# Kernel optimization log

Hardware: AMD Instinct MI355X
Metric: run time of the kernel (lower is better)

## Reference

```python
import jax, jax.numpy as jnp
import numpy as np

DIM_SOL = 8192
DIM_CONTEXT = 2048
DIM_HIDDEN = 4096
INIT = 0.01


def setup_inputs() -> dict:
    key = jax.random.key(0)
    k1, k2, k3, k4, k5, k6 = jax.random.split(key, 6)
    context = jax.random.normal(k1, (DIM_CONTEXT,), dtype=jnp.float32)
    solution = jax.random.randint(k2, (DIM_SOL,), 0, 2).astype(jnp.float32)
    W = jax.random.uniform(k3, (DIM_HIDDEN, DIM_CONTEXT + DIM_SOL), dtype=jnp.float32, minval=-INIT, maxval=INIT)
    U = jax.random.uniform(k4, (DIM_SOL, DIM_HIDDEN), dtype=jnp.float32, minval=-INIT, maxval=INIT)
    b = jax.random.uniform(k5, (DIM_SOL,), dtype=jnp.float32, minval=-INIT, maxval=INIT)
    c = jax.random.uniform(k6, (DIM_HIDDEN,), dtype=jnp.float32, minval=-INIT, maxval=INIT)
    return {"context": context, "solution": solution, "W": W, "U": U, "b": b, "c": c}


def reference(context, solution, W, U, b, c):
    W_ctx = W[:, :DIM_CONTEXT]          # [H, C]
    W_sol = W[:, DIM_CONTEXT:]          # [H, D]
    base = c + W_ctx @ context          # [H]
    # a_i = base + sum_{j<i} W_sol[:, j] * s_j  -> exclusive cumsum over D.
    contrib = W_sol * solution[None, :]                     # [H, D]
    excl = jnp.cumsum(contrib, axis=1) - contrib            # exclusive prefix sum
    A = base[:, None] + excl                                # [H, D]
    H_mat = jax.nn.sigmoid(A.T)                             # [D, H], h at step i
    p_dist = jax.nn.sigmoid(b + jnp.einsum("dh,dh->d", U, H_mat))  # [D]
    # Faithful to source: p_val = prod_i ( p_i^{s_i} + (1 - p_0)^{1 - s_i} )
    terms = jnp.power(p_dist, solution) + jnp.power(1.0 - p_dist[0], 1.0 - solution)
    p_val = jnp.prod(terms)
    return (p_val, p_dist)
```

## Files before the change

### kernel.cpp

```cpp
#include <hip/hip_runtime.h>

#define DSOL 8192
#define DCTX 2048
#define DHID 4096
#define ROWL 10240
#define NSEG 64
#define SEGL 128
#define NCHUNK 16
#define DB 32

typedef float vfloat4 __attribute__((ext_vector_type(4)));

__device__ __forceinline__ float fast_sigmoid(float x) {
    return __builtin_amdgcn_rcpf(1.0f + __expf(-x));
}
__device__ __forceinline__ vfloat4 nt_load4(const float* p) {
    return __builtin_nontemporal_load((const vfloat4*)p);
}

__global__ __launch_bounds__(256) void k_row(
    const float* __restrict__ W, const float* __restrict__ ctx,
    const float* __restrict__ sol, const float* __restrict__ c,
    float* __restrict__ base, float* __restrict__ C)
{
    const int h = blockIdx.x;
    const int t = threadIdx.x;
    const int w = t >> 6, l = t & 63;
    const float* row = W + (size_t)h * ROWL;

    __shared__ float ss[NSEG];
    __shared__ float bred[4];

    float bacc = 0.f;
    #pragma unroll
    for (int i = 0; i < 2; ++i) {
        const int j = i * 1024 + 4 * t;
        const vfloat4 wv = nt_load4(row + j);
        const float4 cv = *(const float4*)(ctx + j);
        bacc += wv.x*cv.x + wv.y*cv.y + wv.z*cv.z + wv.w*cv.w;
    }
    #pragma unroll
    for (int o = 32; o > 0; o >>= 1) bacc += __shfl_xor(bacc, o);
    if (l == 0) bred[w] = bacc;

    const float* rs = row + DCTX;
    #pragma unroll
    for (int i = 0; i < 8; ++i) {
        const int j = i * 1024 + 4 * t;
        const float4 wv = *(const float4*)(rs + j);
        const float4 sv = *(const float4*)(sol + j);
        float a = wv.x*sv.x + wv.y*sv.y + wv.z*sv.z + wv.w*sv.w;
        #pragma unroll
        for (int o = 16; o > 0; o >>= 1) a += __shfl_xor(a, o);
        if ((l & 31) == 0) ss[8*i + 2*w + (l >> 5)] = a;
    }
    __syncthreads();
    if (t == 0) {
        base[h] = c[h] + bred[0] + bred[1] + bred[2] + bred[3];
        float run = 0.f;
        for (int k = 0; k < NSEG; ++k) { const float v = ss[k]; ss[k] = run; run += v; }
    }
    __syncthreads();
    if (t < NSEG) C[t * DHID + h] = ss[t];
}

__global__ __launch_bounds__(256, 4) void k_main(
    const float* __restrict__ W, const float* __restrict__ sol,
    const float* __restrict__ U, const float* __restrict__ base,
    const float* __restrict__ C, float* __restrict__ part)
{
    const int k  = blockIdx.x;
    const int ch = blockIdx.y;
    const int t  = threadIdx.x;
    const int h  = ch * 256 + t;
    const int d0 = k * SEGL;

    __shared__ float T[256][DB + 1];
    __shared__ float sblk[DB];
    __shared__ float R[8][DB];

    float P = C[k * DHID + h];
    const float bs = base[h];

    for (int tb = 0; tb < SEGL / DB; ++tb) {
        const int db0 = d0 + tb * DB;

        {
            int r = t >> 3;
            const int c4 = (t & 7) * 4;
            #pragma unroll
            for (int p = 0; p < 8; ++p, r += 32) {
                const float4 v = *(const float4*)(W + (size_t)(ch*256 + r)*ROWL + DCTX + db0 + c4);
                *(float4*)&T[r][c4] = v;
            }
            if (t < DB) sblk[t] = sol[db0 + t];
        }
        __syncthreads();

        #pragma unroll 8
        for (int d = 0; d < DB; ++d) {
            const float wv = T[t][d];
            const float sg = fast_sigmoid(bs + P);
            const float u  = __builtin_nontemporal_load(U + (size_t)(db0 + d) * DHID + h);
            T[t][d] = u * sg;
            P = fmaf(wv, sblk[d], P);
        }
        __syncthreads();

        {
            const int col = t & 31, g = t >> 5;
            float a = 0.f;
            #pragma unroll
            for (int r = 0; r < 32; ++r) a += T[g*32 + r][col];
            R[g][col] = a;
        }
        __syncthreads();
        if (t < DB) {
            float a = 0.f;
            #pragma unroll
            for (int g = 0; g < 8; ++g) a += R[g][t];
            part[(size_t)ch * DSOL + db0 + t] = a;
        }
        __syncthreads();
    }
}

__global__ __launch_bounds__(256) void k_final(
    const float* __restrict__ b, const float* __restrict__ part,
    const float* __restrict__ sol, float* __restrict__ out,
    float* __restrict__ lsum, float* __restrict__ c0s)
{
    const int t = threadIdx.x;
    const int d = blockIdx.x * 256 + t;
    float acc = b[d];
    #pragma unroll
    for (int cc = 0; cc < NCHUNK; ++cc) acc += part[(size_t)cc * DSOL + d];
    const float p = 1.0f / (1.0f + __expf(-acc));
    out[1 + d] = p;

    const bool one = (sol[d] != 0.0f);
    float lt = one ? __logf(1.0f + p) : 0.0f;
    float c0 = one ? 0.0f : 1.0f;
    #pragma unroll
    for (int o = 32; o > 0; o >>= 1) { lt += __shfl_xor(lt, o); c0 += __shfl_xor(c0, o); }
    __shared__ float rl[4], rc[4];
    if ((t & 63) == 0) { rl[t >> 6] = lt; rc[t >> 6] = c0; }
    __syncthreads();
    if (t == 0) {
        lsum[blockIdx.x] = rl[0] + rl[1] + rl[2] + rl[3];
        c0s [blockIdx.x] = rc[0] + rc[1] + rc[2] + rc[3];
    }
}

__global__ __launch_bounds__(64) void k_tail(
    const float* __restrict__ lsum, const float* __restrict__ c0s,
    float* __restrict__ out)
{
    const int t = threadIdx.x;
    float ls = (t < DSOL/256) ? lsum[t] : 0.0f;
    float c0 = (t < DSOL/256) ? c0s[t]  : 0.0f;
    #pragma unroll
    for (int o = 32; o > 0; o >>= 1) { ls += __shfl_xor(ls, o); c0 += __shfl_xor(c0, o); }
    if (t == 0) {
        const float p0 = out[1];
        const float tot = ls + c0 * __logf(2.0f - p0);
        out[0] = (tot > 88.0f) ? 3.0e38f : __expf(tot);
    }
}

extern "C" void kernel_launch(void* const* d_in, const int* in_sizes, int n_in,
                              void* d_out, int out_size, void* d_ws, size_t ws_size,
                              hipStream_t stream)
{
    const float* ctx = (const float*)d_in[0];
    const float* sol = (const float*)d_in[1];
    const float* W   = (const float*)d_in[2];
    const float* U   = (const float*)d_in[3];
    const float* b   = (const float*)d_in[4];
    const float* c   = (const float*)d_in[5];
    float* out = (float*)d_out;

    float* ws   = (float*)d_ws;
    float* base = ws;
    float* C    = ws + DHID;
    float* part = C + (size_t)NSEG * DHID;
    float* lsum = part + (size_t)NCHUNK * DSOL;
    float* c0s  = lsum + DSOL/256;

    k_row <<<dim3(DHID),         dim3(256), 0, stream>>>(W, ctx, sol, c, base, C);
    k_main<<<dim3(NSEG, NCHUNK), dim3(256), 0, stream>>>(W, sol, U, base, C, part);
    k_final<<<dim3(DSOL / 256),  dim3(256), 0, stream>>>(b, part, sol, out, lsum, c0s);
    k_tail <<<dim3(1),           dim3(64),  0, stream>>>(lsum, c0s, out);
}
```

Measured before the change: 81.11 us.

## Fuse row-prefix kernel into main kernel with per-chunk atomic barrier

Merges the per-row base/segment-prefix computation into the main kernel. Each block computes 4 rows, publishes them, and increments a per-chunk counter. Blocks then spin on the counter until all 64 segments of their chunk are ready. While waiting, each block preloads its first W tile, and later tiles are now prefetched after each step. This removes a kernel launch and overlaps the row pass with tile loads, but it relies on all 1024 blocks being co-resident to avoid deadlock. It also adds a zeroing kernel launch.

```diff
diff --git a/kernel.cpp b/kernel.cpp
--- a/kernel.cpp
+++ b/kernel.cpp
@@ -9,99 +9,103 @@
 #define NCHUNK 16
 #define DB 32
 
-typedef float vfloat4 __attribute__((ext_vector_type(4)));
-
 __device__ __forceinline__ float fast_sigmoid(float x) {
     return __builtin_amdgcn_rcpf(1.0f + __expf(-x));
 }
-__device__ __forceinline__ vfloat4 nt_load4(const float* p) {
-    return __builtin_nontemporal_load((const vfloat4*)p);
-}
-
-__global__ __launch_bounds__(256) void k_row(
+
+__global__ void k_zero(int* __restrict__ cnt) { cnt[threadIdx.x] = 0; }
+
+__global__ __launch_bounds__(256, 4) void k_fused(
     const float* __restrict__ W, const float* __restrict__ ctx,
     const float* __restrict__ sol, const float* __restrict__ c,
-    float* __restrict__ base, float* __restrict__ C)
-{
-    const int h = blockIdx.x;
-    const int t = threadIdx.x;
-    const int w = t >> 6, l = t & 63;
-    const float* row = W + (size_t)h * ROWL;
-
-    __shared__ float ss[NSEG];
-    __shared__ float bred[4];
-
-    float bacc = 0.f;
-    #pragma unroll
-    for (int i = 0; i < 2; ++i) {
-        const int j = i * 1024 + 4 * t;
-        const vfloat4 wv = nt_load4(row + j);
-        const float4 cv = *(const float4*)(ctx + j);
-        bacc += wv.x*cv.x + wv.y*cv.y + wv.z*cv.z + wv.w*cv.w;
-    }
-    #pragma unroll
-    for (int o = 32; o > 0; o >>= 1) bacc += __shfl_xor(bacc, o);
-    if (l == 0) bred[w] = bacc;
-
-    const float* rs = row + DCTX;
-    #pragma unroll
-    for (int i = 0; i < 8; ++i) {
-        const int j = i * 1024 + 4 * t;
-        const float4 wv = *(const float4*)(rs + j);
-        const float4 sv = *(const float4*)(sol + j);
-        float a = wv.x*sv.x + wv.y*sv.y + wv.z*sv.z + wv.w*sv.w;
-        #pragma unroll
-        for (int o = 16; o > 0; o >>= 1) a += __shfl_xor(a, o);
-        if ((l & 31) == 0) ss[8*i + 2*w + (l >> 5)] = a;
-    }
-    __syncthreads();
-    if (t == 0) {
-        base[h] = c[h] + bred[0] + bred[1] + bred[2] + bred[3];
-        float run = 0.f;
-        for (int k = 0; k < NSEG; ++k) { const float v = ss[k]; ss[k] = run; run += v; }
-    }
-    __syncthreads();
-    if (t < NSEG) C[t * DHID + h] = ss[t];
-}
-
-__global__ __launch_bounds__(256, 4) void k_main(
-    const float* __restrict__ W, const float* __restrict__ sol,
-    const float* __restrict__ U, const float* __restrict__ base,
-    const float* __restrict__ C, float* __restrict__ part)
+    const float* __restrict__ U,
+    float* __restrict__ base, float* __restrict__ C,
+    float* __restrict__ part, int* __restrict__ cnt)
 {
     const int k  = blockIdx.x;
     const int ch = blockIdx.y;
     const int t  = threadIdx.x;
-    const int h  = ch * 256 + t;
-    const int d0 = k * SEGL;
-
+    const int w  = t >> 6, l = t & 63;
+
+    __shared__ float ss[4][NSEG];
     __shared__ float T[256][DB + 1];
     __shared__ float sblk[DB];
     __shared__ float R[8][DB];
 
-    float P = C[k * DHID + h];
-    const float bs = base[h];
+    {
+        const int h = ch * 256 + 4 * k + w;
+        const float* row = W + (size_t)h * ROWL;
+
+        float bacc = 0.f;
+        #pragma unroll
+        for (int i = 0; i < 8; ++i) {
+            const int j = i * 256 + l * 4;
+            const float4 wv = *(const float4*)(row + j);
+            const float4 cv = *(const float4*)(ctx + j);
+            bacc += wv.x*cv.x + wv.y*cv.y + wv.z*cv.z + wv.w*cv.w;
+        }
+        #pragma unroll
+        for (int o = 32; o > 0; o >>= 1) bacc += __shfl_xor(bacc, o);
+
+        const float* rs = row + DCTX;
+        #pragma unroll 4
+        for (int g = 0; g < 32; ++g) {
+            const int j = g * 256 + l * 4;
+            const float4 wv = *(const float4*)(rs + j);
+            const float4 sv = *(const float4*)(sol + j);
+            float a = wv.x*sv.x + wv.y*sv.y + wv.z*sv.z + wv.w*sv.w;
+            #pragma unroll
+            for (int o = 16; o > 0; o >>= 1) a += __shfl_xor(a, o);
+            if ((l & 31) == 0) ss[w][2*g + (l >> 5)] = a;
+        }
+        __syncthreads();
+
+        float v = ss[w][l];
+        const float orig = v;
+        #pragma unroll
+        for (int o = 1; o < 64; o <<= 1) {
+            const float u = __shfl_up(v, o);
+            if (l >= o) v += u;
+        }
+        C[(size_t)l * DHID + h] = v - orig;
+        if (l == 0) base[h] = c[h] + bacc;
+    }
+    __threadfence();
+    __syncthreads();
+    if (t == 0)
+        __hip_atomic_fetch_add(&cnt[ch], 1, __ATOMIC_RELEASE, __HIP_MEMORY_SCOPE_AGENT);
+
+    const int h2 = ch * 256 + t;
+    const int d0 = k * SEGL;
+    {
+        int r = t >> 3;
+        const int c4 = (t & 7) * 4;
+        #pragma unroll
+        for (int p = 0; p < 8; ++p, r += 32) {
+            const float4 v = *(const float4*)(W + (size_t)(ch*256 + r)*ROWL + DCTX + d0 + c4);
+            *(float4*)&T[r][c4] = v;
+        }
+        if (t < DB) sblk[t] = sol[d0 + t];
+    }
+
+    for (int spin = 0; spin < (1 << 24); ++spin) {
+        if (__hip_atomic_load(&cnt[ch], __ATOMIC_ACQUIRE, __HIP_MEMORY_SCOPE_AGENT) >= NSEG)
+            break;
+        __builtin_amdgcn_s_sleep(2);
+    }
+    __syncthreads();
+
+    float P = C[(size_t)k * DHID + h2];
+    const float bs = base[h2];
 
     for (int tb = 0; tb < SEGL / DB; ++tb) {
         const int db0 = d0 + tb * DB;
-
-        {
-            int r = t >> 3;
-            const int c4 = (t & 7) * 4;
-            #pragma unroll
-            for (int p = 0; p < 8; ++p, r += 32) {
-                const float4 v = *(const float4*)(W + (size_t)(ch*256 + r)*ROWL + DCTX + db0 + c4);
-                *(float4*)&T[r][c4] = v;
-            }
-            if (t < DB) sblk[t] = sol[db0 + t];
-        }
-        __syncthreads();
 
         #pragma unroll 8
         for (int d = 0; d < DB; ++d) {
             const float wv = T[t][d];
             const float sg = fast_sigmoid(bs + P);
-            const float u  = __builtin_nontemporal_load(U + (size_t)(db0 + d) * DHID + h);
+            const float u  = __builtin_nontemporal_load(U + (size_t)(db0 + d) * DHID + h2);
             T[t][d] = u * sg;
             P = fmaf(wv, sblk[d], P);
         }
@@ -115,11 +119,23 @@
             R[g][col] = a;
         }
         __syncthreads();
+
         if (t < DB) {
             float a = 0.f;
             #pragma unroll
             for (int g = 0; g < 8; ++g) a += R[g][t];
             part[(size_t)ch * DSOL + db0 + t] = a;
+        }
+        if (tb + 1 < SEGL / DB) {
+            const int nb0 = d0 + (tb + 1) * DB;
+            int r = t >> 3;
+            const int c4 = (t & 7) * 4;
+            #pragma unroll
+            for (int p = 0; p < 8; ++p, r += 32) {
+                const float4 v = *(const float4*)(W + (size_t)(ch*256 + r)*ROWL + DCTX + nb0 + c4);
+                *(float4*)&T[r][c4] = v;
+            }
+            if (t < DB) sblk[t] = sol[nb0 + t];
         }
         __syncthreads();
     }
@@ -180,15 +196,16 @@
     const float* c   = (const float*)d_in[5];
     float* out = (float*)d_out;
 
-    float* ws   = (float*)d_ws;
-    float* base = ws;
-    float* C    = ws + DHID;
+    int*   cnt  = (int*)d_ws;
+    float* fws  = (float*)d_ws + 64;
+    float* base = fws;
+    float* C    = base + DHID;
     float* part = C + (size_t)NSEG * DHID;
     float* lsum = part + (size_t)NCHUNK * DSOL;
     float* c0s  = lsum + DSOL/256;
 
-    k_row <<<dim3(DHID),         dim3(256), 0, stream>>>(W, ctx, sol, c, base, C);
-    k_main<<<dim3(NSEG, NCHUNK), dim3(256), 0, stream>>>(W, sol, U, base, C, part);
-    k_final<<<dim3(DSOL / 256),  dim3(256), 0, stream>>>(b, part, sol, out, lsum, c0s);
-    k_tail <<<dim3(1),           dim3(64),  0, stream>>>(lsum, c0s, out);
-}
+    k_zero <<<dim3(1),            dim3(NCHUNK), 0, stream>>>(cnt);
+    k_fused<<<dim3(NSEG, NCHUNK), dim3(256),    0, stream>>>(W, ctx, sol, c, U, base, C, part, cnt);
+    k_final<<<dim3(DSOL / 256),   dim3(256),    0, stream>>>(b, part, sol, out, lsum, c0s);
+    k_tail <<<dim3(1),            dim3(64),     0, stream>>>(lsum, c0s, out);
+}
```

After: 279.6 us. 3.45x slower.
